# Performance work log

Hardware: AMD Instinct MI355X
Metric: run time of the kernel (lower is better)

The kernel has to match this reference:

```python
import jax, jax.numpy as jnp
import numpy as np

B, N, C, H, D = 1, 4096, 256, 8, 64  # batch, seq, channels, heads, head_dim


def setup_inputs() -> dict:
    key = jax.random.key(0)
    ks = jax.random.split(key, 11)
    s = 0.02
    return {
        "q_x": jax.random.normal(ks[0], (B, N, C), jnp.float32),
        "k_x": jax.random.normal(ks[1], (B, N, C), jnp.float32),
        "v_x": jax.random.normal(ks[2], (B, N, C), jnp.float32),
        "bias": jax.random.normal(ks[3], (B, 1, N, N), jnp.float32),
        "wq": jax.random.normal(ks[4], (H * D, C), jnp.float32) * s,
        "wk": jax.random.normal(ks[5], (H * D, C), jnp.float32) * s,
        "wv": jax.random.normal(ks[6], (H * D, C), jnp.float32) * s,
        "wg": jax.random.normal(ks[7], (H * D, C), jnp.float32) * s,
        "bg": jnp.ones((H * D,), jnp.float32),  # gating bias init = 1
        "wo": jax.random.normal(ks[8], (C, H * D), jnp.float32) * s,
        "bo": jnp.zeros((C,), jnp.float32),
        "q_chunk_size": 256,
        "kv_chunk_size": 1024,
    }


def reference(q_x, k_x, v_x, bias, wq, wk, wv, wg, bg, wo, bo,
              q_chunk_size, kv_chunk_size):
    # The chunked Rabe-Staats loop computes exact softmax attention; the
    # chunk sizes are memory knobs only, so the reference computes the
    # mathematically identical full attention.
    q = (q_x @ wq.T).reshape(*q_x.shape[:-1], H, D) / jnp.sqrt(jnp.asarray(D, q_x.dtype))
    k = (k_x @ wk.T).reshape(*k_x.shape[:-1], H, D)
    v = (v_x @ wv.T).reshape(*v_x.shape[:-1], H, D)
    logits = jnp.einsum("bqhd,bkhd->bhqk", q, k) + bias  # [B,H,Q,K]
    p = jax.nn.softmax(logits, axis=-1)
    o = jnp.einsum("bkhd,bhqk->bqhd", v, p)  # [B,Q,H,D]
    g = jax.nn.sigmoid(q_x @ wg.T + bg).reshape(*q_x.shape[:-1], H, D)
    o = o * g
    o = o.reshape(*o.shape[:-2], H * D)
    return o @ wo.T + bo
```

## Files before the change

### kernel.cpp

```cpp
#include <hip/hip_runtime.h>
#include <stdint.h>

#define NN 4096
#define CC 256
#define HD 512
#define DD 64
#define KSPLIT 3

typedef __attribute__((ext_vector_type(8))) short short8;
typedef __attribute__((ext_vector_type(4))) float floatx4;

__device__ __forceinline__ unsigned short f2bf(float x) {
    union { float f; unsigned int u; } v; v.f = x;
    unsigned int u = v.u + 0x7fffu + ((v.u >> 16) & 1u);
    return (unsigned short)(u >> 16);
}
__device__ __forceinline__ float bf2f(unsigned short s) {
    union { unsigned int u; float f; } v; v.u = ((unsigned int)s) << 16;
    return v.f;
}

#if defined(__has_builtin) && __has_builtin(__builtin_amdgcn_cvt_pk_bf16_f32)
typedef __attribute__((ext_vector_type(2))) __bf16 bf16x2_t;
__device__ __forceinline__ unsigned int pack2bf(float a, float b) {
    union { bf16x2_t v; unsigned int u; } x;
    x.v = __builtin_amdgcn_cvt_pk_bf16_f32(a, b);
    return x.u;
}
#else
__device__ __forceinline__ unsigned int pack2bf(float a, float b) {
    return ((unsigned int)f2bf(b) << 16) | (unsigned int)f2bf(a);
}
#endif

#define GLOAD_LDS(gp, lp) __builtin_amdgcn_global_load_lds(                    \
    (__attribute__((address_space(1))) void*)(gp),                             \
    (__attribute__((address_space(3))) void*)(lp), 16, 0, 0)

__global__ __launch_bounds__(256) void prep_kernel(
    const float* __restrict__ qx, const float* __restrict__ kx,
    const float* __restrict__ vx,
    const float* __restrict__ wq, const float* __restrict__ wk,
    const float* __restrict__ wv, const float* __restrict__ wg,
    const float* __restrict__ wo,
    unsigned short* __restrict__ qxb, unsigned short* __restrict__ kxb,
    unsigned short* __restrict__ vxb, unsigned short* __restrict__ Wb,
    unsigned short* __restrict__ wob)
{
    const int z = blockIdx.y;
    const float* src; unsigned short* dst; int n; float s = 1.0f;
    switch (z) {
        case 0: src = qx; dst = qxb; n = NN * CC; break;
        case 1: src = kx; dst = kxb; n = NN * CC; break;
        case 2: src = vx; dst = vxb; n = NN * CC; break;
        case 3: src = wq; dst = Wb;               n = HD * CC; s = 0.125f; break;
        case 4: src = wk; dst = Wb + 1 * HD * CC; n = HD * CC; break;
        case 5: src = wv; dst = Wb + 2 * HD * CC; n = HD * CC; break;
        case 6: src = wg; dst = Wb + 3 * HD * CC; n = HD * CC; break;
        default: src = wo; dst = wob;             n = CC * HD; break;
    }
    int i = (blockIdx.x * 256 + threadIdx.x) * 4;
    if (i < n) {
        float4 v = *(const float4*)&src[i];
        ushort4 p;
        p.x = f2bf(v.x * s); p.y = f2bf(v.y * s);
        p.z = f2bf(v.z * s); p.w = f2bf(v.w * s);
        *(ushort4*)&dst[i] = p;
    }
}

__global__ __launch_bounds__(256, 4) void proj_kernel(
    const unsigned short* __restrict__ qxb, const unsigned short* __restrict__ kxb,
    const unsigned short* __restrict__ vxb, const unsigned short* __restrict__ Wb,
    const float* __restrict__ bg,
    unsigned short* __restrict__ Qb, unsigned short* __restrict__ Kb,
    unsigned short* __restrict__ VbT, unsigned short* __restrict__ Gb)
{
    const int m0 = blockIdx.x * 128;
    const int nb = blockIdx.y;
    const int n0 = nb * 128;
    const int mode = nb >> 2;
    const unsigned short* X = (mode == 1) ? kxb : (mode == 2) ? vxb : qxb;

    const int tid = threadIdx.x;
    const int wid = tid >> 6;
    const int wr = wid >> 1, wc = wid & 1;
    const int lane = tid & 63;
    const int quad = lane >> 4;
    const int ln = lane & 15;
    const int lnx = ln & 7;

    __shared__ __align__(16) unsigned short smem[128 * 136];
    unsigned short* Xs = smem;
    unsigned short* Ws = smem + 128 * 64;

    floatx4 acc[4][4] = {};

    for (int k0 = 0; k0 < CC; k0 += 64) {
        #pragma unroll
        for (int t = 0; t < 4; t++) {
            int row = wid * 32 + t * 8 + (lane >> 3);
            int c = (lane & 7) ^ (lane >> 3);
            GLOAD_LDS(&X[(size_t)(m0 + row) * CC + k0 + c * 8],
                      &Xs[(wid * 32 + t * 8) * 64]);
            GLOAD_LDS(&Wb[(size_t)(n0 + row) * CC + k0 + c * 8],
                      &Ws[(wid * 32 + t * 8) * 64]);
        }
        __syncthreads();

        #pragma unroll
        for (int ks = 0; ks < 64; ks += 32) {
            const int cb = ks >> 3;
            short8 a[4], b[4];
            #pragma unroll
            for (int i = 0; i < 4; i++)
                a[i] = *(const short8*)&Xs[(wr * 64 + i * 16 + ln) * 64 +
                                           (((quad ^ cb) ^ lnx) * 8)];
            #pragma unroll
            for (int j = 0; j < 4; j++)
                b[j] = *(const short8*)&Ws[(wc * 64 + j * 16 + ln) * 64 +
                                           (((quad ^ cb) ^ lnx) * 8)];
            #pragma unroll
            for (int i = 0; i < 4; i++)
                #pragma unroll
                for (int j = 0; j < 4; j++)
                    acc[i][j] = __builtin_amdgcn_mfma_f32_16x16x32_bf16(a[i], b[j], acc[i][j], 0, 0, 0);
        }
        __syncthreads();
    }

    const int subn = nb & 3;
    if (mode != 2) {
        unsigned short* Out = (mode == 0) ? Qb : (mode == 1) ? Kb : Gb;
        #pragma unroll
        for (int i = 0; i < 4; i++) {
            #pragma unroll
            for (int j = 0; j < 4; j++) {
                int col = subn * 128 + wc * 64 + j * 16 + ln;
                float bgv = (mode == 3) ? bg[col] : 0.0f;
                #pragma unroll
                for (int r = 0; r < 4; r++) {
                    int row = m0 + wr * 64 + i * 16 + quad * 4 + r;
                    float v = acc[i][j][r];
                    if (mode == 3) v = 1.0f / (1.0f + __expf(-(v + bgv)));
                    Out[(size_t)row * HD + col] = f2bf(v);
                }
            }
        }
    } else {
        #pragma unroll
        for (int i = 0; i < 4; i++) {
            #pragma unroll
            for (int j = 0; j < 4; j++) {
                int cl = wc * 64 + j * 16 + ln;
                #pragma unroll
                for (int r = 0; r < 4; r++) {
                    int rl = wr * 64 + i * 16 + quad * 4 + r;
                    smem[cl * 136 + rl] = f2bf(acc[i][j][r]);
                }
            }
        }
        __syncthreads();
        #pragma unroll
        for (int it = 0; it < 8; it++) {
            int idx = it * 256 + tid;
            int c = idx >> 4, ch = idx & 15;
            short8 vv = *(const short8*)&smem[c * 136 + ch * 8];
            *(short8*)&VbT[(size_t)(subn * 128 + c) * NN + m0 + ch * 8] = vv;
        }
    }
}

__global__ __launch_bounds__(256, 6) void attn_kernel(
    const unsigned short* __restrict__ Qb, const unsigned short* __restrict__ Kb,
    const unsigned short* __restrict__ VbT,
    const float* __restrict__ bias,
    unsigned short* __restrict__ Opart, float* __restrict__ Lpart)
{
    const int h = blockIdx.y;
    const int q0 = blockIdx.x * 64;
    const int sp = blockIdx.z;
    const int tbeg = (sp * 64) / KSPLIT;
    const int tend = ((sp + 1) * 64) / KSPLIT;
    const int tid = threadIdx.x;
    const int wid = tid >> 6;
    const int lane = tid & 63;
    const int quad = lane >> 4;
    const int ln = lane & 15;
    const int lnx = ln & 7;

    __shared__ __align__(16) unsigned short Ks[64 * 64];
    __shared__ __align__(16) unsigned short Vs[64 * 64];
    __shared__ __align__(16) unsigned short Ps[64 * 72];

    const int qrow = q0 + wid * 16 + ln;
    short8 qa0 = *(const short8*)&Qb[(size_t)qrow * HD + h * DD + quad * 8];
    short8 qa1 = *(const short8*)&Qb[(size_t)qrow * HD + h * DD + 32 + quad * 8];

    floatx4 O[4] = {};
    float lsum[4] = {0.0f, 0.0f, 0.0f, 0.0f};

    for (int kt = tbeg; kt < tend; kt++) {
        const int k0 = kt * 64;
        #pragma unroll
        for (int t = 0; t < 2; t++) {
            int row = wid * 16 + t * 8 + (lane >> 3);
            int c = (lane & 7) ^ (lane >> 3);
            GLOAD_LDS(&Kb[(size_t)(k0 + row) * HD + h * DD + c * 8],
                      &Ks[(wid * 16 + t * 8) * 64]);
            GLOAD_LDS(&VbT[(size_t)(h * DD + row) * NN + k0 + c * 8],
                      &Vs[(wid * 16 + t * 8) * 64]);
        }

        float bv[4][4];
        #pragma unroll
        for (int r = 0; r < 4; r++) {
            const float* brow = &bias[(size_t)(q0 + wid * 16 + quad * 4 + r) * NN + k0];
            #pragma unroll
            for (int n = 0; n < 4; n++) bv[r][n] = brow[n * 16 + ln];
        }
        __syncthreads();

        floatx4 S[4];
        #pragma unroll
        for (int n = 0; n < 4; n++)
            S[n] = (floatx4){bv[0][n], bv[1][n], bv[2][n], bv[3][n]};
        #pragma unroll
        for (int n = 0; n < 4; n++) {
            short8 b0 = *(const short8*)&Ks[(n * 16 + ln) * 64 + ((quad ^ lnx) * 8)];
            S[n] = __builtin_amdgcn_mfma_f32_16x16x32_bf16(qa0, b0, S[n], 0, 0, 0);
            short8 b1 = *(const short8*)&Ks[(n * 16 + ln) * 64 + (((quad ^ 4) ^ lnx) * 8)];
            S[n] = __builtin_amdgcn_mfma_f32_16x16x32_bf16(qa1, b1, S[n], 0, 0, 0);
        }

        #pragma unroll
        for (int r = 0; r < 4; r++) {
            int prow = (wid * 16 + quad * 4 + r) * 72;
            #pragma unroll
            for (int n = 0; n < 4; n += 2) {
                float p0 = __expf(S[n][r]);
                float p1 = __expf(S[n + 1][r]);
                lsum[r] += p0 + p1;
                unsigned int pk = pack2bf(p0, p1);
                Ps[prow + n * 16 + ln] = (unsigned short)(pk & 0xffffu);
                Ps[prow + (n + 1) * 16 + ln] = (unsigned short)(pk >> 16);
            }
        }

        #pragma unroll
        for (int ks = 0; ks < 64; ks += 32) {
            const int cb = ks >> 3;
            short8 a = *(const short8*)&Ps[(wid * 16 + ln) * 72 + ks + quad * 8];
            #pragma unroll
            for (int nd = 0; nd < 4; nd++) {
                short8 b = *(const short8*)&Vs[(nd * 16 + ln) * 64 +
                                               (((quad ^ cb) ^ lnx) * 8)];
                O[nd] = __builtin_amdgcn_mfma_f32_16x16x32_bf16(a, b, O[nd], 0, 0, 0);
            }
        }
        __syncthreads();
    }

    #pragma unroll
    for (int r = 0; r < 4; r++) {
        #pragma unroll
        for (int off = 1; off < 16; off <<= 1)
            lsum[r] += __shfl_xor(lsum[r], off);
        int grow = q0 + wid * 16 + quad * 4 + r;
        size_t base = ((size_t)(sp * 8 + h) * NN + grow) * 64;
        #pragma unroll
        for (int nd = 0; nd < 4; nd++)
            Opart[base + nd * 16 + ln] = f2bf(O[nd][r]);
        if (ln == 0)
            Lpart[(size_t)(sp * 8 + h) * NN + grow] = lsum[r];
    }
}

__global__ __launch_bounds__(256) void combine_kernel(
    const unsigned short* __restrict__ Opart, const float* __restrict__ Lpart,
    const unsigned short* __restrict__ Gb, unsigned short* __restrict__ OGb)
{
    const int tid = threadIdx.x;
    const int d = tid & 63;
    const int flat = blockIdx.x * 4 + (tid >> 6);
    const int h = flat >> 12;
    const int q = flat & (NN - 1);

    float l = 0.0f, o = 0.0f;
    #pragma unroll
    for (int sp = 0; sp < KSPLIT; sp++) {
        size_t idx = (size_t)(sp * 8 + h) * NN + q;
        l += Lpart[idx];
        o += bf2f(Opart[idx * 64 + d]);
    }
    float inv = 1.0f / l;
    int col = h * DD + d;
    float g = bf2f(Gb[(size_t)q * HD + col]);
    OGb[(size_t)q * HD + col] = f2bf(o * inv * g);
}

__global__ __launch_bounds__(256, 4) void outproj_kernel(
    const unsigned short* __restrict__ OGb, const unsigned short* __restrict__ wob,
    const float* __restrict__ bo, float* __restrict__ out)
{
    const int m0 = blockIdx.x * 64;
    const int n0 = blockIdx.y * 64;
    const int tid = threadIdx.x;
    const int wid = tid >> 6;
    const int lane = tid & 63;
    const int quad = lane >> 4;
    const int ln = lane & 15;
    const int lnx = ln & 7;

    __shared__ __align__(16) unsigned short Xs[64 * 64];
    __shared__ __align__(16) unsigned short Ws[64 * 64];

    floatx4 acc[4] = {};

    for (int k0 = 0; k0 < HD; k0 += 64) {
        #pragma unroll
        for (int t = 0; t < 2; t++) {
            int row = wid * 16 + t * 8 + (lane >> 3);
            int c = (lane & 7) ^ (lane >> 3);
            GLOAD_LDS(&OGb[(size_t)(m0 + row) * HD + k0 + c * 8],
                      &Xs[(wid * 16 + t * 8) * 64]);
            GLOAD_LDS(&wob[(size_t)(n0 + row) * HD + k0 + c * 8],
                      &Ws[(wid * 16 + t * 8) * 64]);
        }
        __syncthreads();

        #pragma unroll
        for (int ks = 0; ks < 64; ks += 32) {
            const int cb = ks >> 3;
            short8 a = *(const short8*)&Xs[(wid * 16 + ln) * 64 +
                                           (((quad ^ cb) ^ lnx) * 8)];
            #pragma unroll
            for (int n = 0; n < 4; n++) {
                short8 b = *(const short8*)&Ws[(n * 16 + ln) * 64 +
                                               (((quad ^ cb) ^ lnx) * 8)];
                acc[n] = __builtin_amdgcn_mfma_f32_16x16x32_bf16(a, b, acc[n], 0, 0, 0);
            }
        }
        __syncthreads();
    }

    #pragma unroll
    for (int n = 0; n < 4; n++) {
        int col = n0 + n * 16 + ln;
        float bov = bo[col];
        #pragma unroll
        for (int r = 0; r < 4; r++) {
            int row = m0 + wid * 16 + quad * 4 + r;
            out[(size_t)row * CC + col] = acc[n][r] + bov;
        }
    }
}

extern "C" void kernel_launch(void* const* d_in, const int* in_sizes, int n_in,
                              void* d_out, int out_size, void* d_ws, size_t ws_size,
                              hipStream_t stream) {
    const float* qx   = (const float*)d_in[0];
    const float* kx   = (const float*)d_in[1];
    const float* vx   = (const float*)d_in[2];
    const float* bias = (const float*)d_in[3];
    const float* wq   = (const float*)d_in[4];
    const float* wk   = (const float*)d_in[5];
    const float* wv   = (const float*)d_in[6];
    const float* wg   = (const float*)d_in[7];
    const float* bg   = (const float*)d_in[8];
    const float* wo   = (const float*)d_in[9];
    const float* bo   = (const float*)d_in[10];
    float* out = (float*)d_out;

    char* ws = (char*)d_ws;
    const size_t MB = (size_t)1 << 20;
    unsigned short* wob   = (unsigned short*)(ws);
    float*          Lpart = (float*)(ws + MB / 4);
    unsigned short* Qb    = (unsigned short*)(ws + 1 * MB);
    unsigned short* Kb    = (unsigned short*)(ws + 5 * MB);
    unsigned short* VbT   = (unsigned short*)(ws + 9 * MB);
    unsigned short* Gb    = (unsigned short*)(ws + 13 * MB);
    unsigned short* OGb   = (unsigned short*)(ws + 17 * MB);
    unsigned short* qxb   = (unsigned short*)(ws + 21 * MB);
    unsigned short* kxb   = (unsigned short*)(ws + 23 * MB);
    unsigned short* vxb   = (unsigned short*)(ws + 25 * MB);
    unsigned short* Wb    = (unsigned short*)(ws + 27 * MB);
    unsigned short* Opart = (unsigned short*)(ws + 21 * MB);

    prep_kernel<<<dim3(NN * CC / (256 * 4), 8), 256, 0, stream>>>(
        qx, kx, vx, wq, wk, wv, wg, wo, qxb, kxb, vxb, Wb, wob);
    proj_kernel<<<dim3(32, 16), 256, 0, stream>>>(
        qxb, kxb, vxb, Wb, bg, Qb, Kb, VbT, Gb);
    attn_kernel<<<dim3(64, 8, KSPLIT), 256, 0, stream>>>(
        Qb, Kb, VbT, bias, Opart, Lpart);
    combine_kernel<<<dim3(NN * 8 / 4), 256, 0, stream>>>(
        Opart, Lpart, Gb, OGb);
    outproj_kernel<<<dim3(64, 4), 256, 0, stream>>>(
        OGb, wob, bo, out);
}
```

Before: 210.8 us.

## Double-buffer LDS tiles in projection and output-projection GEMMs

Converts the proj and outproj GEMM main loops to a two-stage LDS pipeline: the next K-tile is issued as a global-to-LDS load before the current tile's MFMAs run. The aim is to hide global load latency behind compute. Shared memory per block doubles and the launch-bounds occupancy hint drops from 4 to 2. The visible hunks do not show where the end-of-iteration barrier sits after the new prefetch, so correctness depends on lines that are not shown. Most of the runtime is in the attention kernel, which only gains an unused variable.

```diff
diff --git a/kernel.cpp b/kernel.cpp
--- a/kernel.cpp
+++ b/kernel.cpp
@@ -69,7 +69,7 @@
     }
 }
 
-__global__ __launch_bounds__(256, 4) void proj_kernel(
+__global__ __launch_bounds__(256, 2) void proj_kernel(
     const unsigned short* __restrict__ qxb, const unsigned short* __restrict__ kxb,
     const unsigned short* __restrict__ vxb, const unsigned short* __restrict__ Wb,
     const float* __restrict__ bg,
@@ -90,13 +90,13 @@
     const int ln = lane & 15;
     const int lnx = ln & 7;
 
-    __shared__ __align__(16) unsigned short smem[128 * 136];
-    unsigned short* Xs = smem;
-    unsigned short* Ws = smem + 128 * 64;
+    __shared__ __align__(16) unsigned short smem[4 * 128 * 64];
 
     floatx4 acc[4][4] = {};
 
-    for (int k0 = 0; k0 < CC; k0 += 64) {
+    auto STAGE = [&](int k0, int bf) {
+        unsigned short* Xs = smem + bf * 16384;
+        unsigned short* Ws = smem + bf * 16384 + 8192;
         #pragma unroll
         for (int t = 0; t < 4; t++) {
             int row = wid * 32 + t * 8 + (lane >> 3);
@@ -106,8 +106,17 @@
             GLOAD_LDS(&Wb[(size_t)(n0 + row) * CC + k0 + c * 8],
                       &Ws[(wid * 32 + t * 8) * 64]);
         }
-        __syncthreads();
-
+    };
+
+    STAGE(0, 0);
+    __syncthreads();
+
+    for (int it = 0; it < 4; it++) {
+        const int bf = it & 1;
+        if (it + 1 < 4) STAGE((it + 1) * 64, bf ^ 1);
+
+        const unsigned short* Xs = smem + bf * 16384;
+        const unsigned short* Ws = smem + bf * 16384 + 8192;
         #pragma unroll
         for (int ks = 0; ks < 64; ks += 32) {
             const int cb = ks >> 3;
@@ -188,6 +197,7 @@
     const int quad = lane >> 4;
     const int ln = lane & 15;
     const int lnx = ln & 7;
+    const int sc = (lane & 7) ^ (lane >> 3);
 
     __shared__ __align__(16) unsigned short Ks[64 * 64];
     __shared__ __align__(16) unsigned short Vs[64 * 64];
@@ -299,7 +309,7 @@
     OGb[(size_t)q * HD + col] = f2bf(o * inv * g);
 }
 
-__global__ __launch_bounds__(256, 4) void outproj_kernel(
+__global__ __launch_bounds__(256, 2) void outproj_kernel(
     const unsigned short* __restrict__ OGb, const unsigned short* __restrict__ wob,
     const float* __restrict__ bo, float* __restrict__ out)
 {
@@ -312,32 +322,39 @@
     const int ln = lane & 15;
     const int lnx = ln & 7;
 
-    __shared__ __align__(16) unsigned short Xs[64 * 64];
-    __shared__ __align__(16) unsigned short Ws[64 * 64];
+    __shared__ __align__(16) unsigned short Xs[2][64 * 64];
+    __shared__ __align__(16) unsigned short Ws[2][64 * 64];
 
     floatx4 acc[4] = {};
 
-    for (int k0 = 0; k0 < HD; k0 += 64) {
+    auto STAGE = [&](int k0, int bf) {
         #pragma unroll
         for (int t = 0; t < 2; t++) {
             int row = wid * 16 + t * 8 + (lane >> 3);
             int c = (lane & 7) ^ (lane >> 3);
             GLOAD_LDS(&OGb[(size_t)(m0 + row) * HD + k0 + c * 8],
-                      &Xs[(wid * 16 + t * 8) * 64]);
+                      &Xs[bf][(wid * 16 + t * 8) * 64]);
             GLOAD_LDS(&wob[(size_t)(n0 + row) * HD + k0 + c * 8],
-                      &Ws[(wid * 16 + t * 8) * 64]);
-        }
-        __syncthreads();
+                      &Ws[bf][(wid * 16 + t * 8) * 64]);
+        }
+    };
+
+    STAGE(0, 0);
+    __syncthreads();
+
+    for (int it = 0; it < 8; it++) {
+        const int bf = it & 1;
+        if (it + 1 < 8) STAGE((it + 1) * 64, bf ^ 1);
 
         #pragma unroll
         for (int ks = 0; ks < 64; ks += 32) {
             const int cb = ks >> 3;
-            short8 a = *(const short8*)&Xs[(wid * 16 + ln) * 64 +
-                                           (((quad ^ cb) ^ lnx) * 8)];
+            short8 a = *(const short8*)&Xs[bf][(wid * 16 + ln) * 64 +
+                                              (((quad ^ cb) ^ lnx) * 8)];
             #pragma unroll
             for (int n = 0; n < 4; n++) {
-                short8 b = *(const short8*)&Ws[(n * 16 + ln) * 64 +
-                                               (((quad ^ cb) ^ lnx) * 8)];
+                short8 b = *(const short8*)&Ws[bf][(n * 16 + ln) * 64 +
+                                                   (((quad ^ cb) ^ lnx) * 8)];
                 acc[n] = __builtin_amdgcn_mfma_f32_16x16x32_bf16(a, b, acc[n], 0, 0, 0);
             }
         }
```

New measurement: 209.2 us. Within noise of the previous version (-0.8%).

## Shrink projection and out-projection tiles, double-buffer out-projection loads

Applied to the files above, without the earlier changes.

The projection GEMM moves from 128x128 tiles (512 blocks) to 64x64 tiles (2048 blocks), and the out-projection from 64x64 to 32x64 tiles (512 blocks) with a double-buffered LDS prefetch of the next K slice. The aim is to fill the many CUs on the device better and hide global-load latency in the out-projection. In exchange, data reuse per block drops and operand traffic to L2 grows.

```diff
diff --git a/kernel.cpp b/kernel.cpp
--- a/kernel.cpp
+++ b/kernel.cpp
@@ -69,104 +69,91 @@
     }
 }
 
-__global__ __launch_bounds__(256, 4) void proj_kernel(
+__global__ __launch_bounds__(256, 8) void proj_kernel(
     const unsigned short* __restrict__ qxb, const unsigned short* __restrict__ kxb,
     const unsigned short* __restrict__ vxb, const unsigned short* __restrict__ Wb,
     const float* __restrict__ bg,
     unsigned short* __restrict__ Qb, unsigned short* __restrict__ Kb,
     unsigned short* __restrict__ VbT, unsigned short* __restrict__ Gb)
 {
-    const int m0 = blockIdx.x * 128;
+    const int m0 = blockIdx.x * 64;
     const int nb = blockIdx.y;
-    const int n0 = nb * 128;
-    const int mode = nb >> 2;
+    const int mode = nb >> 3;
+    const int subn = nb & 7;
+    const int n0 = mode * HD + subn * 64;
     const unsigned short* X = (mode == 1) ? kxb : (mode == 2) ? vxb : qxb;
 
     const int tid = threadIdx.x;
     const int wid = tid >> 6;
-    const int wr = wid >> 1, wc = wid & 1;
     const int lane = tid & 63;
     const int quad = lane >> 4;
     const int ln = lane & 15;
     const int lnx = ln & 7;
 
-    __shared__ __align__(16) unsigned short smem[128 * 136];
+    __shared__ __align__(16) unsigned short smem[2 * 64 * 64];
     unsigned short* Xs = smem;
-    unsigned short* Ws = smem + 128 * 64;
-
-    floatx4 acc[4][4] = {};
+    unsigned short* Ws = smem + 64 * 64;
+
+    floatx4 acc[4] = {};
 
     for (int k0 = 0; k0 < CC; k0 += 64) {
         #pragma unroll
-        for (int t = 0; t < 4; t++) {
-            int row = wid * 32 + t * 8 + (lane >> 3);
+        for (int t = 0; t < 2; t++) {
+            int row = wid * 16 + t * 8 + (lane >> 3);
             int c = (lane & 7) ^ (lane >> 3);
             GLOAD_LDS(&X[(size_t)(m0 + row) * CC + k0 + c * 8],
-                      &Xs[(wid * 32 + t * 8) * 64]);
+                      &Xs[(wid * 16 + t * 8) * 64]);
             GLOAD_LDS(&Wb[(size_t)(n0 + row) * CC + k0 + c * 8],
-                      &Ws[(wid * 32 + t * 8) * 64]);
+                      &Ws[(wid * 16 + t * 8) * 64]);
         }
         __syncthreads();
 
         #pragma unroll
         for (int ks = 0; ks < 64; ks += 32) {
             const int cb = ks >> 3;
-            short8 a[4], b[4];
-            #pragma unroll
-            for (int i = 0; i < 4; i++)
-                a[i] = *(const short8*)&Xs[(wr * 64 + i * 16 + ln) * 64 +
+            short8 a = *(const short8*)&Xs[(wid * 16 + ln) * 64 +
                                            (((quad ^ cb) ^ lnx) * 8)];
             #pragma unroll
-            for (int j = 0; j < 4; j++)
-                b[j] = *(const short8*)&Ws[(wc * 64 + j * 16 + ln) * 64 +
-                                           (((quad ^ cb) ^ lnx) * 8)];
-            #pragma unroll
-            for (int i = 0; i < 4; i++)
-                #pragma unroll
-                for (int j = 0; j < 4; j++)
-                    acc[i][j] = __builtin_amdgcn_mfma_f32_16x16x32_bf16(a[i], b[j], acc[i][j], 0, 0, 0);
-        }
-        __syncthreads();
-    }
-
-    const int subn = nb & 3;
+            for (int n = 0; n < 4; n++) {
+                short8 b = *(const short8*)&Ws[(n * 16 + ln) * 64 +
+                                               (((quad ^ cb) ^ lnx) * 8)];
+                acc[n] = __builtin_amdgcn_mfma_f32_16x16x32_bf16(a, b, acc[n], 0, 0, 0);
+            }
+        }
+        __syncthreads();
+    }
+
     if (mode != 2) {
         unsigned short* Out = (mode == 0) ? Qb : (mode == 1) ? Kb : Gb;
         #pragma unroll
-        for (int i = 0; i < 4; i++) {
-            #pragma unroll
-            for (int j = 0; j < 4; j++) {
-                int col = subn * 128 + wc * 64 + j * 16 + ln;
-                float bgv = (mode == 3) ? bg[col] : 0.0f;
-                #pragma unroll
-                for (int r = 0; r < 4; r++) {
-                    int row = m0 + wr * 64 + i * 16 + quad * 4 + r;
-                    float v = acc[i][j][r];
-                    if (mode == 3) v = 1.0f / (1.0f + __expf(-(v + bgv)));
-                    Out[(size_t)row * HD + col] = f2bf(v);
-                }
+        for (int n = 0; n < 4; n++) {
+            int col = subn * 64 + n * 16 + ln;
+            float bgv = (mode == 3) ? bg[col] : 0.0f;
+            #pragma unroll
+            for (int r = 0; r < 4; r++) {
+                int row = m0 + wid * 16 + quad * 4 + r;
+                float v = acc[n][r];
+                if (mode == 3) v = 1.0f / (1.0f + __expf(-(v + bgv)));
+                Out[(size_t)row * HD + col] = f2bf(v);
             }
         }
     } else {
         #pragma unroll
-        for (int i = 0; i < 4; i++) {
-            #pragma unroll
-            for (int j = 0; j < 4; j++) {
-                int cl = wc * 64 + j * 16 + ln;
-                #pragma unroll
-                for (int r = 0; r < 4; r++) {
-                    int rl = wr * 64 + i * 16 + quad * 4 + r;
-                    smem[cl * 136 + rl] = f2bf(acc[i][j][r]);
-                }
-            }
-        }
-        __syncthreads();
-        #pragma unroll
-        for (int it = 0; it < 8; it++) {
+        for (int n = 0; n < 4; n++) {
+            int cl = n * 16 + ln;
+            #pragma unroll
+            for (int r = 0; r < 4; r++) {
+                int rl = wid * 16 + quad * 4 + r;
+                smem[cl * 72 + rl] = f2bf(acc[n][r]);
+            }
+        }
+        __syncthreads();
+        #pragma unroll
+        for (int it = 0; it < 2; it++) {
             int idx = it * 256 + tid;
-            int c = idx >> 4, ch = idx & 15;
-            short8 vv = *(const short8*)&smem[c * 136 + ch * 8];
-            *(short8*)&VbT[(size_t)(subn * 128 + c) * NN + m0 + ch * 8] = vv;
+            int c = idx >> 3, ch = idx & 7;
+            short8 vv = *(const short8*)&smem[c * 72 + ch * 8];
+            *(short8*)&VbT[(size_t)(subn * 64 + c) * NN + m0 + ch * 8] = vv;
         }
     }
 }
@@ -299,59 +286,68 @@
     OGb[(size_t)q * HD + col] = f2bf(o * inv * g);
 }
 
-__global__ __launch_bounds__(256, 4) void outproj_kernel(
+__global__ __launch_bounds__(256, 2) void outproj_kernel(
     const unsigned short* __restrict__ OGb, const unsigned short* __restrict__ wob,
     const float* __restrict__ bo, float* __restrict__ out)
 {
-    const int m0 = blockIdx.x * 64;
+    const int m0 = blockIdx.x * 32;
     const int n0 = blockIdx.y * 64;
     const int tid = threadIdx.x;
     const int wid = tid >> 6;
+    const int wr = wid >> 1, wc = wid & 1;
     const int lane = tid & 63;
     const int quad = lane >> 4;
     const int ln = lane & 15;
     const int lnx = ln & 7;
 
-    __shared__ __align__(16) unsigned short Xs[64 * 64];
-    __shared__ __align__(16) unsigned short Ws[64 * 64];
-
-    floatx4 acc[4] = {};
-
-    for (int k0 = 0; k0 < HD; k0 += 64) {
+    __shared__ __align__(16) unsigned short Xs[2][32 * 64];
+    __shared__ __align__(16) unsigned short Ws[2][64 * 64];
+
+    floatx4 acc[2] = {};
+
+    auto STAGE = [&](int k0, int bf) {
+        int c = (lane & 7) ^ (lane >> 3);
+        int xrow = wid * 8 + (lane >> 3);
+        GLOAD_LDS(&OGb[(size_t)(m0 + xrow) * HD + k0 + c * 8],
+                  &Xs[bf][(wid * 8) * 64]);
         #pragma unroll
         for (int t = 0; t < 2; t++) {
-            int row = wid * 16 + t * 8 + (lane >> 3);
-            int c = (lane & 7) ^ (lane >> 3);
-            GLOAD_LDS(&OGb[(size_t)(m0 + row) * HD + k0 + c * 8],
-                      &Xs[(wid * 16 + t * 8) * 64]);
-            GLOAD_LDS(&wob[(size_t)(n0 + row) * HD + k0 + c * 8],
-                      &Ws[(wid * 16 + t * 8) * 64]);
-        }
-        __syncthreads();
+            int wrow = wid * 16 + t * 8 + (lane >> 3);
+            GLOAD_LDS(&wob[(size_t)(n0 + wrow) * HD + k0 + c * 8],
+                      &Ws[bf][(wid * 16 + t * 8) * 64]);
+        }
+    };
+
+    STAGE(0, 0);
+    __syncthreads();
+
+    for (int it = 0; it < 8; it++) {
+        const int bf = it & 1;
+        if (it + 1 < 8) STAGE((it + 1) * 64, bf ^ 1);
 
         #pragma unroll
         for (int ks = 0; ks < 64; ks += 32) {
             const int cb = ks >> 3;
-            short8 a = *(const short8*)&Xs[(wid * 16 + ln) * 64 +
-                                           (((quad ^ cb) ^ lnx) * 8)];
-            #pragma unroll
-            for (int n = 0; n < 4; n++) {
-                short8 b = *(const short8*)&Ws[(n * 16 + ln) * 64 +
-                                               (((quad ^ cb) ^ lnx) * 8)];
-                acc[n] = __builtin_amdgcn_mfma_f32_16x16x32_bf16(a, b, acc[n], 0, 0, 0);
+            short8 a = *(const short8*)&Xs[bf][(wr * 16 + ln) * 64 +
+                                              (((quad ^ cb) ^ lnx) * 8)];
+            #pragma unroll
+            for (int j = 0; j < 2; j++) {
+                short8 b = *(const short8*)&Ws[bf][(wc * 32 + j * 16 + ln) * 64 +
+                                                   (((quad ^ cb) ^ lnx) * 8)];
+                acc[j] = __builtin_amdgcn_mfma_f32_16x16x32_bf16(a, b, acc[j], 0, 0, 0);
             }
         }
         __syncthreads();
     }
 
     #pragma unroll
-    for (int n = 0; n < 4; n++) {
-        int col = n0 + n * 16 + ln;
+    for (int j = 0; j < 2; j++) {
+        int col = n0 + wc * 32 + j * 16 + ln;
         float bov = bo[col];
         #pragma unroll
         for (int r = 0; r < 4; r++) {
-            int row = m0 + wid * 16 + quad * 4 + r;
-            out[(size_t)row * CC + col] = acc[n][r] + bov;
+            int row = m0 + wr * 16 + quad * 4 + r;
+            out[(size_t)row * CC + col] = acc[j][r] + bov;
         }
     }
 }
@@ -389,12 +385,12 @@
 
     prep_kernel<<<dim3(NN * CC / (256 * 4), 8), 256, 0, stream>>>(
         qx, kx, vx, wq, wk, wv, wg, wo, qxb, kxb, vxb, Wb, wob);
-    proj_kernel<<<dim3(32, 16), 256, 0, stream>>>(
+    proj_kernel<<<dim3(64, 32), 256, 0, stream>>>(
         qxb, kxb, vxb, Wb, bg, Qb, Kb, VbT, Gb);
     attn_kernel<<<dim3(64, 8, KSPLIT), 256, 0, stream>>>(
         Qb, Kb, VbT, bias, Opart, Lpart);
     combine_kernel<<<dim3(NN * 8 / 4), 256, 0, stream>>>(
         Opart, Lpart, Gb, OGb);
-    outproj_kernel<<<dim3(64, 4), 256, 0, stream>>>(
+    outproj_kernel<<<dim3(128, 4), 256, 0, stream>>>(
         OGb, wob, bo, out);
 }
```

Measured after the change: 209.7 us. About the same (-0.5%).
